# Optimization experiments

Measured on AMD Instinct MI355X. Metric: run time of the kernel, lower is better.

The kernel has to match this reference:

```python
import jax, jax.numpy as jnp
import numpy as np
import math

N_HEADS = 16
D_HEAD = 128
D_ROPE = 32
SPLIT = D_HEAD - D_ROPE  # 96
LATENT = 512
D_MODEL = 2048
B, T = 2, 2048


def _rotary_emb(num_tokens, d_rope):
    inv_freq = 1.0 / (10000.0 ** (jnp.arange(0, d_rope, 2, dtype=jnp.float32) / d_rope))
    t = jnp.arange(num_tokens, dtype=jnp.float32)
    freqs = jnp.einsum('t,f->tf', t, inv_freq)          # [T, d_rope/2]
    return jnp.concatenate([freqs, freqs], axis=-1)      # [T, d_rope]


def _apply_rotary(x, cos, sin):
    # x: [B,T,H,d_rope]; cos/sin: [1,T,1,d_rope]
    half = x.shape[-1] // 2
    x1, x2 = x[..., :half], x[..., half:]
    rot = jnp.concatenate([-x2, x1], axis=-1)
    return x * cos + rot * sin


def setup_inputs() -> dict:
    key = jax.random.key(0)
    ks = jax.random.split(key, 20)
    s = 0.02
    def w(k, i, o):
        return jax.random.normal(k, (i, o), dtype=jnp.float32) * s
    inp = {
        'input': jax.random.normal(ks[0], (B, T, D_MODEL), dtype=jnp.float32),
        'batch_size': B,
        'num_tokens': T,
        'Wdkv_w': w(ks[1], D_MODEL, LATENT), 'Wdkv_b': jnp.zeros((LATENT,), jnp.float32),
        'Wdq_w':  w(ks[2], D_MODEL, LATENT), 'Wdq_b':  jnp.zeros((LATENT,), jnp.float32),
        'Wuk_w':  w(ks[3], LATENT, N_HEADS * SPLIT),  'Wuk_b': jnp.zeros((N_HEADS * SPLIT,), jnp.float32),
        'Wuv_w':  w(ks[4], LATENT, N_HEADS * D_HEAD), 'Wuv_b': jnp.zeros((N_HEADS * D_HEAD,), jnp.float32),
        'Wuq_w':  w(ks[5], LATENT, N_HEADS * SPLIT),  'Wuq_b': jnp.zeros((N_HEADS * SPLIT,), jnp.float32),
        'Wqr_w':  w(ks[6], LATENT, N_HEADS * D_ROPE), 'Wqr_b': jnp.zeros((N_HEADS * D_ROPE,), jnp.float32),
        'Wkr_w':  w(ks[7], D_MODEL, N_HEADS * D_ROPE), 'Wkr_b': jnp.zeros((N_HEADS * D_ROPE,), jnp.float32),
        'Wo_w':   w(ks[8], N_HEADS * D_HEAD, D_MODEL), 'Wo_b': jnp.zeros((D_MODEL,), jnp.float32),
    }
    return inp


def reference(input, batch_size, num_tokens,
              Wdkv_w, Wdkv_b, Wdq_w, Wdq_b, Wuk_w, Wuk_b, Wuv_w, Wuv_b,
              Wuq_w, Wuq_b, Wqr_w, Wqr_b, Wkr_w, Wkr_b, Wo_w, Wo_b):
    lin = lambda x, w, b: x @ w + b
    bsz, T_ = batch_size, num_tokens

    c_kv = lin(input, Wdkv_w, Wdkv_b)                                   # [B,T,latent]
    k_base = lin(c_kv, Wuk_w, Wuk_b).reshape(bsz, T_, N_HEADS, SPLIT)
    v = lin(c_kv, Wuv_w, Wuv_b).reshape(bsz, T_, N_HEADS, D_HEAD)

    c_q = lin(input, Wdq_w, Wdq_b)
    q_base = lin(c_q, Wuq_w, Wuq_b).reshape(bsz, T_, N_HEADS, SPLIT)
    q_rot = lin(c_q, Wqr_w, Wqr_b).reshape(bsz, T_, N_HEADS, D_ROPE)

    emb = _rotary_emb(T_, D_ROPE)                                        # [T,d_rope]
    cos = jnp.cos(emb)[None, :, None, :]
    sin = jnp.sin(emb)[None, :, None, :]
    q_rot = _apply_rotary(q_rot, cos, sin)
    k_rot = _apply_rotary(lin(input, Wkr_w, Wkr_b).reshape(bsz, T_, N_HEADS, D_ROPE), cos, sin)

    q = jnp.concatenate([q_base, q_rot], axis=-1)                        # [B,T,H,d_head]
    k = jnp.concatenate([k_base, k_rot], axis=-1)

    scores = jnp.einsum('bqhd,bkhd->bhqk', q, k) / math.sqrt(D_HEAD)
    attn = jax.nn.softmax(scores, axis=-1)
    out = jnp.einsum('bhqk,bkhd->bqhd', attn, v)
    out = lin(out.reshape(bsz, T_, N_HEADS * D_HEAD), Wo_w, Wo_b)
    return out, c_kv, k_rot
```

## Files before the change

kernel.cpp:

```cpp
#include <hip/hip_runtime.h>

typedef __bf16 bf16x8 __attribute__((ext_vector_type(8)));
typedef float f32x4 __attribute__((ext_vector_type(4)));
typedef float f32x16 __attribute__((ext_vector_type(16)));

#define NROWS 4096
#define DM 2048
#define LAT 512
#define NH 16
#define DH 128

__device__ __forceinline__ unsigned short f2bf(float f) {
    union { float f; unsigned u; } v; v.f = f;
    unsigned r = v.u + 0x7fffu + ((v.u >> 16) & 1u);
    return (unsigned short)(r >> 16);
}
__device__ __forceinline__ void gload16(const void* g, void* l) {
    __builtin_amdgcn_global_load_lds((const __attribute__((address_space(1))) unsigned int*)g,
                                     (__attribute__((address_space(3))) unsigned int*)l, 16, 0, 0);
}
__device__ __forceinline__ unsigned cvtpk_bf16(float lo, float hi) {
    unsigned r;
    asm("v_cvt_pk_bf16_f32 %0, %1, %2" : "=v"(r) : "v"(lo), "v"(hi));
    return r;
}
__device__ __forceinline__ void pl32swap(unsigned& a, unsigned& b) {
    asm("v_permlane32_swap_b32 %0, %1" : "+v"(a), "+v"(b));
}
__device__ __forceinline__ float exp2a(float x) {
    float r;
    asm("v_exp_f32 %0, %1" : "=v"(r) : "v"(x));
    return r;
}

struct PrepParams {
    const float* tsrc[8]; unsigned short* tdst[8];
    int tK[8]; int tN[8]; int tstart[8];
    const float* input; unsigned short* xbf;
    float* cs; float* sn;
    const float* bsrc[8]; float* bdst[8]; int blen[8];
};

#define PREP_T_END   9984
#define PREP_X_END   18176
#define PREP_R_END   18304
#define PREP_B_END   18340

__global__ __launch_bounds__(256) void prep_kernel(PrepParams P) {
    const int bid = blockIdx.x, tid = threadIdx.x;
    if (bid < PREP_T_END) {
        int j = 0;
        #pragma unroll
        for (int i = 1; i < 8; ++i) if (bid >= P.tstart[i]) j = i;
        const int local = bid - P.tstart[j];
        const float* W = P.tsrc[j];
        unsigned short* Wt = P.tdst[j];
        const int K = P.tK[j], N = P.tN[j];
        const int nbx = N >> 5;
        const int nb = (local % nbx) * 32, kb = (local / nbx) * 32;
        __shared__ float tile[32][33];
        const int tx = tid & 31, ty = tid >> 5;
        #pragma unroll
        for (int i = 0; i < 32; i += 8)
            tile[ty + i][tx] = W[(size_t)(kb + ty + i) * N + nb + tx];
        __syncthreads();
        #pragma unroll
        for (int i = 0; i < 32; i += 8)
            Wt[(size_t)(nb + ty + i) * K + kb + tx] = f2bf(tile[tx][ty + i]);
    } else if (bid < PREP_X_END) {
        const int i = ((bid - PREP_T_END) * 256 + tid) * 4;
        float4 v = *(const float4*)(P.input + i);
        unsigned short* y = P.xbf + i;
        y[0] = f2bf(v.x); y[1] = f2bf(v.y); y[2] = f2bf(v.z); y[3] = f2bf(v.w);
    } else if (bid < PREP_R_END) {
        const int idx = (bid - PREP_X_END) * 256 + tid;
        const int i = idx & 15, t = idx >> 4;
        float inv = powf(10000.0f, -(float)i / 16.0f);
        float a = (float)t * inv;
        P.cs[idx] = cosf(a);
        P.sn[idx] = sinf(a);
    } else {
        const int gid = (bid - PREP_R_END) * 256 + tid;
        int off = 0;
        #pragma unroll
        for (int i = 0; i < 8; ++i) {
            if (gid >= off && gid < off + P.blen[i])
                P.bdst[i][gid - off] = P.bsrc[i][gid - off];
            off += P.blen[i];
        }
    }
}

__global__ __launch_bounds__(256) void gemm_fused_kernel(const unsigned short* __restrict__ A,
                                                         const unsigned short* __restrict__ Bt,
                                                         const float* __restrict__ biascat,
                                                         int K, int which,
                                                         float* __restrict__ outF,
                                                         unsigned short* __restrict__ outB0,
                                                         unsigned short* __restrict__ outB1,
                                                         unsigned short* __restrict__ outB0k,
                                                         float* __restrict__ outRope,
                                                         const float* __restrict__ cs,
                                                         const float* __restrict__ sn) {
    __shared__ __align__(16) unsigned short SM[2][8192];
    const int tid = threadIdx.x;
    const int mb = blockIdx.x * 128;
    const int by = blockIdx.y, nb = by * 128;
    const int w = tid >> 6, lane = tid & 63;
    const int wr = (w >> 1) * 64, wc = (w & 1) * 64;
    const int l15 = lane & 15, l4 = lane >> 4;
    const int srow = lane >> 2, sko = (lane & 3) * 8;

    f32x4 acc[4][4] = {};

    auto STAGE = [&](int buf, int k0) {
        #pragma unroll
        for (int c = 0; c < 16; c += 4) {
            int cc = c + w;
            if (cc < 8)
                gload16(A + (size_t)(mb + cc * 16 + srow) * K + k0 + sko, SM[buf] + cc * 512);
            else
                gload16(Bt + (size_t)(nb + (cc - 8) * 16 + srow) * K + k0 + sko, SM[buf] + 4096 + (cc - 8) * 512);
        }
    };

    const int nk = K >> 5;
    STAGE(0, 0);
    for (int kt = 0; kt < nk; ++kt) {
        const int buf = kt & 1;
        if (kt + 1 < nk) {
            STAGE(buf ^ 1, (kt + 1) << 5);
            asm volatile("s_waitcnt vmcnt(4)" ::: "memory");
        } else {
            asm volatile("s_waitcnt vmcnt(0)" ::: "memory");
        }
        __builtin_amdgcn_sched_barrier(0);
        __builtin_amdgcn_s_barrier();
        __builtin_amdgcn_sched_barrier(0);

        const unsigned short* As = SM[buf];
        const unsigned short* Bs = SM[buf] + 4096;
        bf16x8 af[4], bfr[4];
        #pragma unroll
        for (int mi = 0; mi < 4; ++mi)
            af[mi] = *(const bf16x8*)(As + (wr + mi * 16 + l15) * 32 + l4 * 8);
        #pragma unroll
        for (int ni = 0; ni < 4; ++ni)
            bfr[ni] = *(const bf16x8*)(Bs + (wc + ni * 16 + l15) * 32 + l4 * 8);
        #pragma unroll
        for (int mi = 0; mi < 4; ++mi)
            #pragma unroll
            for (int ni = 0; ni < 4; ++ni)
                acc[mi][ni] = __builtin_amdgcn_mfma_f32_16x16x32_bf16(af[mi], bfr[ni], acc[mi][ni], 0, 0, 0);
        __builtin_amdgcn_s_barrier();
    }

    if (which == 1 && by >= 12) {
        unsigned short* BT = &SM[0][0];
        const int c2b = nb - 1536;
        #pragma unroll
        for (int half = 0; half < 2; ++half) {
            __syncthreads();
            if ((wr >> 6) == half) {
                #pragma unroll
                for (int mi = 0; mi < 4; ++mi)
                    #pragma unroll
                    for (int ni = 0; ni < 4; ++ni) {
                        const int col = wc + ni * 16 + l15;
                        const float bv = biascat[nb + col];
                        ushort4 pv;
                        pv.x = f2bf(acc[mi][ni][0] + bv);
                        pv.y = f2bf(acc[mi][ni][1] + bv);
                        pv.z = f2bf(acc[mi][ni][2] + bv);
                        pv.w = f2bf(acc[mi][ni][3] + bv);
                        *(ushort4*)(BT + col * 72 + mi * 16 + l4 * 4) = pv;
                    }
            }
            __syncthreads();
            const int c = tid >> 1;
            #pragma unroll
            for (int j = 0; j < 4; ++j) {
                const int seg = (tid & 1) * 4 + j;
                uint4 val = *(const uint4*)(BT + c * 72 + seg * 8);
                *(uint4*)(outB1 + (size_t)(c2b + c) * 4096 + mb + half * 64 + seg * 8) = val;
            }
        }
        return;
    }

    #pragma unroll
    for (int mi = 0; mi < 4; ++mi) {
        const int row0 = mb + wr + mi * 16 + l4 * 4;
        #pragma unroll
        for (int ni = 0; ni < 4; ++ni) {
            const int colg = nb + wc + ni * 16 + l15;
            const float bv = biascat[colg];
            float v[4];
            #pragma unroll
            for (int r = 0; r < 4; ++r) v[r] = acc[mi][ni][r] + bv;

            if (which == 0) {
                if (by < 4) {
                    #pragma unroll
                    for (int r = 0; r < 4; ++r) {
                        outF[(size_t)(row0 + r) * 512 + colg] = v[r];
                        outB0[(size_t)(row0 + r) * 512 + colg] = f2bf(v[r]);
                    }
                } else if (by < 8) {
                    const int c2 = colg - 512;
                    #pragma unroll
                    for (int r = 0; r < 4; ++r)
                        outB1[(size_t)(row0 + r) * 512 + c2] = f2bf(v[r]);
                } else {
                    const int cloc = colg - 1024, i2 = cloc & 31, h2 = cloc >> 5;
                    const float pbv = biascat[colg ^ 16];
                    const bool lo = (ni & 1) == 0;
                    #pragma unroll
                    for (int r = 0; r < 4; ++r) {
                        float vp = acc[mi][ni ^ 1][r] + pbv;
                        int t = (row0 + r) & 2047;
                        float cc_ = cs[t * 16 + (i2 & 15)], ss_ = sn[t * 16 + (i2 & 15)];
                        float o = lo ? (v[r] * cc_ - vp * ss_) : (v[r] * cc_ + vp * ss_);
                        outRope[(size_t)(row0 + r) * 512 + cloc] = o;
                        outB0k[(size_t)(row0 + r) * 2048 + h2 * 128 + 96 + i2] = f2bf(o);
                    }
                }
            } else if (which == 1) {
                const int ocol = (colg / 96) * 128 + colg % 96;
                #pragma unroll
                for (int r = 0; r < 4; ++r)
                    outB0[(size_t)(row0 + r) * 2048 + ocol] = f2bf(v[r]);
            } else if (which == 2) {
                if (by < 12) {
                    const int ocol = (colg / 96) * 128 + colg % 96;
                    #pragma unroll
                    for (int r = 0; r < 4; ++r)
                        outB0[(size_t)(row0 + r) * 2048 + ocol] = f2bf(v[r]);
                } else {
                    const int cloc = colg - 1536, i2 = cloc & 31, h2 = cloc >> 5;
                    const float pbv = biascat[colg ^ 16];
                    const bool lo = (ni & 1) == 0;
                    #pragma unroll
                    for (int r = 0; r < 4; ++r) {
                        float vp = acc[mi][ni ^ 1][r] + pbv;
                        int t = (row0 + r) & 2047;
                        float cc_ = cs[t * 16 + (i2 & 15)], ss_ = sn[t * 16 + (i2 & 15)];
                        float o = lo ? (v[r] * cc_ - vp * ss_) : (v[r] * cc_ + vp * ss_);
                        outB0[(size_t)(row0 + r) * 2048 + h2 * 128 + 96 + i2] = f2bf(o);
                    }
                }
            } else {
                #pragma unroll
                for (int r = 0; r < 4; ++r)
                    outF[(size_t)(row0 + r) * 2048 + colg] = v[r];
            }
        }
    }
}

__global__ __launch_bounds__(256, 2) void attn_kernel(const unsigned short* __restrict__ Q,
                                                      const unsigned short* __restrict__ Kb,
                                                      const unsigned short* __restrict__ Vtg,
                                                      unsigned short* __restrict__ O) {
    __shared__ __align__(16) unsigned short Ks[2][64 * 128];
    __shared__ __align__(16) unsigned short Vs[2][128 * 64];

    const int tid = threadIdx.x, w = tid >> 6, lane = tid & 63;
    const int l31 = lane & 31, hi = lane >> 5;
    const int bid = blockIdx.x;
    const int logical = (bid & 7) * 64 + (bid >> 3);
    const int bh = logical >> 4, b = bh >> 4, h = bh & 15;
    const int qt = (logical & 15) * 128 + w * 32;
    const int qrow = qt + l31;
    const float sl2e = 0.08838834764831845f * 1.4426950408889634f;

    bf16x8 qf[8];
    const unsigned short* qptr = Q + (size_t)(b * 2048 + qrow) * 2048 + h * 128 + hi * 8;
    #pragma unroll
    for (int s = 0; s < 8; ++s) qf[s] = *(const bf16x8*)(qptr + s * 16);

    f32x16 acc[4] = {};
    float m_run = -1e30f, l_run = 0.0f;

    const int kl15 = lane >> 4, kd0 = lane & 15;
    const int vr = lane >> 3, vk = lane & 7;

    auto STAGE = [&](int buf, int kt) {
        #pragma unroll
        for (int i = 0; i < 4; ++i) {
            int c = w * 4 + i;
            int key = c * 4 + kl15;
            int d0 = (kd0 * 8) ^ ((key & 7) << 3);
            gload16(Kb + (size_t)(b * 2048 + kt + key) * 2048 + h * 128 + d0, &Ks[buf][c * 512]);
            int dv = c * 8 + vr;
            int k0 = (vk * 8) ^ ((dv & 7) << 3);
            gload16(Vtg + (size_t)(h * 128 + dv) * 4096 + b * 2048 + kt + k0, &Vs[buf][c * 512]);
        }
    };

    STAGE(0, 0);

    for (int t = 0; t < 32; ++t) {
        const int buf = t & 1;
        if (t < 31) {
            STAGE(buf ^ 1, (t + 1) * 64);
            asm volatile("s_waitcnt vmcnt(8)" ::: "memory");
        } else {
            asm volatile("s_waitcnt vmcnt(0)" ::: "memory");
        }
        __builtin_amdgcn_sched_barrier(0);
        __builtin_amdgcn_s_barrier();
        __builtin_amdgcn_sched_barrier(0);

        #pragma unroll
        for (int g = 0; g < 2; ++g) {
            const int key = g * 32 + l31;
            const unsigned short* kbase = &Ks[buf][key * 128];
            const int ksw = (key & 7) << 3;
            f32x16 sc = {};
            __builtin_amdgcn_s_setprio(1);
            #pragma unroll
            for (int s = 0; s < 8; ++s) {
                bf16x8 kf = *(const bf16x8*)(kbase + ((s * 16 + hi * 8) ^ ksw));
                sc = __builtin_amdgcn_mfma_f32_32x32x16_bf16(kf, qf[s], sc, 0, 0, 0);
            }
            __builtin_amdgcn_s_setprio(0);

            float t0 = fmaxf(sc[0], sc[1]),  t1 = fmaxf(sc[2], sc[3]);
            float t2 = fmaxf(sc[4], sc[5]),  t3 = fmaxf(sc[6], sc[7]);
            float t4 = fmaxf(sc[8], sc[9]),  t5 = fmaxf(sc[10], sc[11]);
            float t6 = fmaxf(sc[12], sc[13]), t7 = fmaxf(sc[14], sc[15]);
            float pm = fmaxf(fmaxf(fmaxf(t0, t1), fmaxf(t2, t3)),
                             fmaxf(fmaxf(t4, t5), fmaxf(t6, t7)));
            pm = fmaxf(pm, __shfl_xor(pm, 32, 64));

            if (__any(pm > m_run + 90.51f)) {
                float mn = fmaxf(m_run, pm);
                float f = exp2a((m_run - mn) * sl2e);
                m_run = mn;
                l_run *= f;
                #pragma unroll
                for (int dg = 0; dg < 4; ++dg)
                    #pragma unroll
                    for (int i = 0; i < 16; ++i) acc[dg][i] *= f;
            }
            const float mexp2 = m_run * sl2e;

            float e[16];
            #pragma unroll
            for (int j = 0; j < 16; ++j)
                e[j] = exp2a(fmaf(sc[j], sl2e, -mexp2));
            float a0 = e[0] + e[1], a1 = e[2] + e[3], a2 = e[4] + e[5], a3 = e[6] + e[7];
            float a4 = e[8] + e[9], a5 = e[10] + e[11], a6 = e[12] + e[13], a7 = e[14] + e[15];
            l_run += ((a0 + a1) + (a2 + a3)) + ((a4 + a5) + (a6 + a7));

            #pragma unroll
            for (int s2 = 0; s2 < 2; ++s2) {
                unsigned X0 = cvtpk_bf16(e[s2 * 8 + 0], e[s2 * 8 + 1]);
                unsigned X1 = cvtpk_bf16(e[s2 * 8 + 2], e[s2 * 8 + 3]);
                unsigned Y0 = cvtpk_bf16(e[s2 * 8 + 4], e[s2 * 8 + 5]);
                unsigned Y1 = cvtpk_bf16(e[s2 * 8 + 6], e[s2 * 8 + 7]);
                pl32swap(X0, Y0);
                pl32swap(X1, Y1);
                union { unsigned u[4]; bf16x8 v; } pf;
                pf.u[0] = X0; pf.u[1] = X1; pf.u[2] = Y0; pf.u[3] = Y1;

                const int kofs = g * 32 + s2 * 16 + hi * 8;
                __builtin_amdgcn_s_setprio(1);
                #pragma unroll
                for (int dg = 0; dg < 4; ++dg) {
                    const int d = dg * 32 + l31;
                    bf16x8 vf = *(const bf16x8*)(&Vs[buf][d * 64 + (kofs ^ ((d & 7) << 3))]);
                    acc[dg] = __builtin_amdgcn_mfma_f32_32x32x16_bf16(vf, pf.v, acc[dg], 0, 0, 0);
                }
                __builtin_amdgcn_s_setprio(0);
            }
        }
        __builtin_amdgcn_s_barrier();
    }

    l_run += __shfl_xor(l_run, 32, 64);
    const float inv = 1.0f / l_run;
    unsigned short* obase = O + (size_t)(b * 2048 + qrow) * 2048 + h * 128;
    #pragma unroll
    for (int dg = 0; dg < 4; ++dg)
        #pragma unroll
        for (int k = 0; k < 4; ++k) {
            ushort4 pv;
            pv.x = f2bf(acc[dg][4 * k + 0] * inv);
            pv.y = f2bf(acc[dg][4 * k + 1] * inv);
            pv.z = f2bf(acc[dg][4 * k + 2] * inv);
            pv.w = f2bf(acc[dg][4 * k + 3] * inv);
            *(ushort4*)(obase + dg * 32 + k * 8 + hi * 4) = pv;
        }
}

extern "C" void kernel_launch(void* const* d_in, const int* in_sizes, int n_in,
                              void* d_out, int out_size, void* d_ws, size_t ws_size,
                              hipStream_t stream) {
    (void)in_sizes; (void)n_in; (void)out_size; (void)ws_size;

    const float* input  = (const float*)d_in[0];
    const float* Wdkv_w = (const float*)d_in[3];
    const float* Wdkv_b = (const float*)d_in[4];
    const float* Wdq_w  = (const float*)d_in[5];
    const float* Wdq_b  = (const float*)d_in[6];
    const float* Wuk_w  = (const float*)d_in[7];
    const float* Wuk_b  = (const float*)d_in[8];
    const float* Wuv_w  = (const float*)d_in[9];
    const float* Wuv_b  = (const float*)d_in[10];
    const float* Wuq_w  = (const float*)d_in[11];
    const float* Wuq_b  = (const float*)d_in[12];
    const float* Wqr_w  = (const float*)d_in[13];
    const float* Wqr_b  = (const float*)d_in[14];
    const float* Wkr_w  = (const float*)d_in[15];
    const float* Wkr_b  = (const float*)d_in[16];
    const float* Wo_w   = (const float*)d_in[17];
    const float* Wo_b   = (const float*)d_in[18];

    float* out_main = (float*)d_out;
    float* out_ckv  = out_main + (size_t)NROWS * DM;
    float* out_krot = out_ckv + (size_t)NROWS * LAT;

    char* p = (char*)d_ws;
    auto alloc = [&](size_t bytes) { char* r = p; p += (bytes + 255) & ~(size_t)255; return r; };
    unsigned short* x_bf  = (unsigned short*)alloc((size_t)NROWS * DM * 2);
    unsigned short* w1_t  = (unsigned short*)alloc((size_t)1536 * DM * 2);
    unsigned short* w2_t  = (unsigned short*)alloc((size_t)3584 * LAT * 2);
    unsigned short* w3_t  = (unsigned short*)alloc((size_t)2048 * LAT * 2);
    unsigned short* w4_t  = (unsigned short*)alloc((size_t)DM * DM * 2);
    unsigned short* ckv_bf = (unsigned short*)alloc((size_t)NROWS * LAT * 2);
    unsigned short* cq_bf  = (unsigned short*)alloc((size_t)NROWS * LAT * 2);
    unsigned short* q_bf   = (unsigned short*)alloc((size_t)NROWS * DM * 2);
    unsigned short* k_bf   = (unsigned short*)alloc((size_t)NROWS * DM * 2);
    unsigned short* vt_g   = (unsigned short*)alloc((size_t)DM * NROWS * 2);
    unsigned short* ao_bf  = (unsigned short*)alloc((size_t)NROWS * DM * 2);
    float* cos_t = (float*)alloc((size_t)2048 * 16 * 4);
    float* sin_t = (float*)alloc((size_t)2048 * 16 * 4);
    float* bc1 = (float*)alloc(1536 * 4);
    float* bc2 = (float*)alloc(3584 * 4);
    float* bc3 = (float*)alloc(2048 * 4);
    float* bc4 = (float*)alloc(2048 * 4);

    PrepParams P;
    const float* tsrc[8] = {Wdkv_w, Wdq_w, Wkr_w, Wuk_w, Wuv_w, Wuq_w, Wqr_w, Wo_w};
    unsigned short* tdst[8] = {w1_t, w1_t + 512 * 2048, w1_t + 1024 * 2048,
                               w2_t, w2_t + 1536 * 512, w3_t, w3_t + 1536 * 512, w4_t};
    int tK[8] = {2048, 2048, 2048, 512, 512, 512, 512, 2048};
    int tN[8] = {512, 512, 512, 1536, 2048, 1536, 512, 2048};
    int tstart[8] = {0, 1024, 2048, 3072, 3840, 4864, 5632, 5888};
    const float* bsrc[8] = {Wdkv_b, Wdq_b, Wkr_b, Wuk_b, Wuv_b, Wuq_b, Wqr_b, Wo_b};
    float* bdst[8] = {bc1, bc1 + 512, bc1 + 1024, bc2, bc2 + 1536, bc3, bc3 + 1536, bc4};
    int blen[8] = {512, 512, 512, 1536, 2048, 1536, 512, 2048};
    for (int i = 0; i < 8; ++i) {
        P.tsrc[i] = tsrc[i]; P.tdst[i] = tdst[i]; P.tK[i] = tK[i]; P.tN[i] = tN[i];
        P.tstart[i] = tstart[i]; P.bsrc[i] = bsrc[i]; P.bdst[i] = bdst[i]; P.blen[i] = blen[i];
    }
    P.input = input; P.xbf = x_bf; P.cs = cos_t; P.sn = sin_t;
    prep_kernel<<<PREP_B_END, 256, 0, stream>>>(P);

    gemm_fused_kernel<<<dim3(32, 12), 256, 0, stream>>>(x_bf, w1_t, bc1, 2048, 0,
                                                        out_ckv, ckv_bf, cq_bf, k_bf, out_krot, cos_t, sin_t);
    gemm_fused_kernel<<<dim3(32, 28), 256, 0, stream>>>(ckv_bf, w2_t, bc2, 512, 1,
                                                        nullptr, k_bf, vt_g, nullptr, nullptr, nullptr, nullptr);
    gemm_fused_kernel<<<dim3(32, 16), 256, 0, stream>>>(cq_bf, w3_t, bc3, 512, 2,
                                                        nullptr, q_bf, nullptr, nullptr, nullptr, cos_t, sin_t);

    attn_kernel<<<512, 256, 0, stream>>>(q_bf, k_bf, vt_g, ao_bf);

    gemm_fused_kernel<<<dim3(32, 16), 256, 0, stream>>>(ao_bf, w4_t, bc4, 2048, 3,
                                                        out_main, nullptr, nullptr, nullptr, nullptr, nullptr, nullptr);
}
```

Baseline: 240.0 us.

## Merge up-projection GEMMs into one launch and use BK=64 for K=2048 GEMMs

Concatenates the Wuk/Wuv and Wuq/Wqr transposed weights into one buffer so the K- and Q-side up-projections run as a single 44-column-block launch. Blocks past column block 28 read from the c_q activation instead of c_kv. Separately templates the GEMM on BK and uses BK=64 for the K=2048 GEMMs to halve barrier and loop iterations. The merge removes one launch and improves occupancy, at the cost of doubled LDS for the BK=64 instances and more epilogue branching.

Measured after the change: 254.1 us. +5.9%, slower.

```diff
diff --git a/kernel.cpp b/kernel.cpp
--- a/kernel.cpp
+++ b/kernel.cpp
@@ -91,7 +91,9 @@
     }
 }
 
+template<int BK>
 __global__ __launch_bounds__(256) void gemm_fused_kernel(const unsigned short* __restrict__ A,
+                                                         const unsigned short* __restrict__ A2,
                                                          const unsigned short* __restrict__ Bt,
                                                          const float* __restrict__ biascat,
                                                          int K, int which,
@@ -102,35 +104,41 @@
                                                          float* __restrict__ outRope,
                                                          const float* __restrict__ cs,
                                                          const float* __restrict__ sn) {
-    __shared__ __align__(16) unsigned short SM[2][8192];
+    constexpr int RPC = 512 / BK;
+    constexpr int NCHA = BK / 4;
+    __shared__ __align__(16) unsigned short SM[2][256 * BK];
     const int tid = threadIdx.x;
     const int mb = blockIdx.x * 128;
     const int by = blockIdx.y, nb = by * 128;
     const int w = tid >> 6, lane = tid & 63;
     const int wr = (w >> 1) * 64, wc = (w & 1) * 64;
     const int l15 = lane & 15, l4 = lane >> 4;
-    const int srow = lane >> 2, sko = (lane & 3) * 8;
+    const int srow = lane / (BK / 8), sko = (lane % (BK / 8)) * 8;
+
+    const unsigned short* Ause = (which == 1 && by >= 28) ? A2 : A;
 
     f32x4 acc[4][4] = {};
 
     auto STAGE = [&](int buf, int k0) {
         #pragma unroll
-        for (int c = 0; c < 16; c += 4) {
+        for (int c = 0; c < 2 * NCHA; c += 4) {
             int cc = c + w;
-            if (cc < 8)
-                gload16(A + (size_t)(mb + cc * 16 + srow) * K + k0 + sko, SM[buf] + cc * 512);
+            if (cc < NCHA)
+                gload16(Ause + (size_t)(mb + cc * RPC + srow) * K + k0 + sko, SM[buf] + cc * 512);
             else
-                gload16(Bt + (size_t)(nb + (cc - 8) * 16 + srow) * K + k0 + sko, SM[buf] + 4096 + (cc - 8) * 512);
+                gload16(Bt + (size_t)(nb + (cc - NCHA) * RPC + srow) * K + k0 + sko,
+                        SM[buf] + 128 * BK + (cc - NCHA) * 512);
         }
     };
 
-    const int nk = K >> 5;
+    const int nk = K / BK;
     STAGE(0, 0);
     for (int kt = 0; kt < nk; ++kt) {
         const int buf = kt & 1;
         if (kt + 1 < nk) {
-            STAGE(buf ^ 1, (kt + 1) << 5);
-            asm volatile("s_waitcnt vmcnt(4)" ::: "memory");
+            STAGE(buf ^ 1, (kt + 1) * BK);
+            if constexpr (BK == 32) asm volatile("s_waitcnt vmcnt(4)" ::: "memory");
+            else                    asm volatile("s_waitcnt vmcnt(8)" ::: "memory");
         } else {
             asm volatile("s_waitcnt vmcnt(0)" ::: "memory");
         }
@@ -139,23 +147,26 @@
         __builtin_amdgcn_sched_barrier(0);
 
         const unsigned short* As = SM[buf];
-        const unsigned short* Bs = SM[buf] + 4096;
-        bf16x8 af[4], bfr[4];
-        #pragma unroll
-        for (int mi = 0; mi < 4; ++mi)
-            af[mi] = *(const bf16x8*)(As + (wr + mi * 16 + l15) * 32 + l4 * 8);
-        #pragma unroll
-        for (int ni = 0; ni < 4; ++ni)
-            bfr[ni] = *(const bf16x8*)(Bs + (wc + ni * 16 + l15) * 32 + l4 * 8);
-        #pragma unroll
-        for (int mi = 0; mi < 4; ++mi)
+        const unsigned short* Bs = SM[buf] + 128 * BK;
+        #pragma unroll
+        for (int kk = 0; kk < BK; kk += 32) {
+            bf16x8 af[4], bfr[4];
+            #pragma unroll
+            for (int mi = 0; mi < 4; ++mi)
+                af[mi] = *(const bf16x8*)(As + (wr + mi * 16 + l15) * BK + kk + l4 * 8);
             #pragma unroll
             for (int ni = 0; ni < 4; ++ni)
-                acc[mi][ni] = __builtin_amdgcn_mfma_f32_16x16x32_bf16(af[mi], bfr[ni], acc[mi][ni], 0, 0, 0);
+                bfr[ni] = *(const bf16x8*)(Bs + (wc + ni * 16 + l15) * BK + kk + l4 * 8);
+            #pragma unroll
+            for (int mi = 0; mi < 4; ++mi)
+                #pragma unroll
+                for (int ni = 0; ni < 4; ++ni)
+                    acc[mi][ni] = __builtin_amdgcn_mfma_f32_16x16x32_bf16(af[mi], bfr[ni], acc[mi][ni], 0, 0, 0);
+        }
         __builtin_amdgcn_s_barrier();
     }
 
-    if (which == 1 && by >= 12) {
+    if (which == 1 && by >= 12 && by < 28) {
         unsigned short* BT = &SM[0][0];
         const int c2b = nb - 1536;
         #pragma unroll
@@ -226,18 +237,19 @@
                     }
                 }
             } else if (which == 1) {
-                const int ocol = (colg / 96) * 128 + colg % 96;
-                #pragma unroll
-                for (int r = 0; r < 4; ++r)
-                    outB0[(size_t)(row0 + r) * 2048 + ocol] = f2bf(v[r]);
-            } else if (which == 2) {
                 if (by < 12) {
                     const int ocol = (colg / 96) * 128 + colg % 96;
                     #pragma unroll
                     for (int r = 0; r < 4; ++r)
                         outB0[(size_t)(row0 + r) * 2048 + ocol] = f2bf(v[r]);
+                } else if (by < 40) {
+                    const int c3 = colg - 3584;
+                    const int ocol = (c3 / 96) * 128 + c3 % 96;
+                    #pragma unroll
+                    for (int r = 0; r < 4; ++r)
+                        outB0k[(size_t)(row0 + r) * 2048 + ocol] = f2bf(v[r]);
                 } else {
-                    const int cloc = colg - 1536, i2 = cloc & 31, h2 = cloc >> 5;
+                    const int cloc = colg - 5120, i2 = cloc & 31, h2 = cloc >> 5;
                     const float pbv = biascat[colg ^ 16];
                     const bool lo = (ni & 1) == 0;
                     #pragma unroll
@@ -246,7 +258,7 @@
                         int t = (row0 + r) & 2047;
                         float cc_ = cs[t * 16 + (i2 & 15)], ss_ = sn[t * 16 + (i2 & 15)];
                         float o = lo ? (v[r] * cc_ - vp * ss_) : (v[r] * cc_ + vp * ss_);
-                        outB0[(size_t)(row0 + r) * 2048 + h2 * 128 + 96 + i2] = f2bf(o);
+                        outB0k[(size_t)(row0 + r) * 2048 + h2 * 128 + 96 + i2] = f2bf(o);
                     }
                 }
             } else {
@@ -426,8 +438,7 @@
     auto alloc = [&](size_t bytes) { char* r = p; p += (bytes + 255) & ~(size_t)255; return r; };
     unsigned short* x_bf  = (unsigned short*)alloc((size_t)NROWS * DM * 2);
     unsigned short* w1_t  = (unsigned short*)alloc((size_t)1536 * DM * 2);
-    unsigned short* w2_t  = (unsigned short*)alloc((size_t)3584 * LAT * 2);
-    unsigned short* w3_t  = (unsigned short*)alloc((size_t)2048 * LAT * 2);
+    unsigned short* w23_t = (unsigned short*)alloc((size_t)5632 * LAT * 2);
     unsigned short* w4_t  = (unsigned short*)alloc((size_t)DM * DM * 2);
     unsigned short* ckv_bf = (unsigned short*)alloc((size_t)NROWS * LAT * 2);
     unsigned short* cq_bf  = (unsigned short*)alloc((size_t)NROWS * LAT * 2);
@@ -437,20 +448,19 @@
     unsigned short* ao_bf  = (unsigned short*)alloc((size_t)NROWS * DM * 2);
     float* cos_t = (float*)alloc((size_t)2048 * 16 * 4);
     float* sin_t = (float*)alloc((size_t)2048 * 16 * 4);
-    float* bc1 = (float*)alloc(1536 * 4);
-    float* bc2 = (float*)alloc(3584 * 4);
-    float* bc3 = (float*)alloc(2048 * 4);
-    float* bc4 = (float*)alloc(2048 * 4);
+    float* bc1  = (float*)alloc(1536 * 4);
+    float* bc23 = (float*)alloc(5632 * 4);
+    float* bc4  = (float*)alloc(2048 * 4);
 
     PrepParams P;
     const float* tsrc[8] = {Wdkv_w, Wdq_w, Wkr_w, Wuk_w, Wuv_w, Wuq_w, Wqr_w, Wo_w};
     unsigned short* tdst[8] = {w1_t, w1_t + 512 * 2048, w1_t + 1024 * 2048,
-                               w2_t, w2_t + 1536 * 512, w3_t, w3_t + 1536 * 512, w4_t};
+                               w23_t, w23_t + 1536 * 512, w23_t + 3584 * 512, w23_t + 5120 * 512, w4_t};
     int tK[8] = {2048, 2048, 2048, 512, 512, 512, 512, 2048};
     int tN[8] = {512, 512, 512, 1536, 2048, 1536, 512, 2048};
     int tstart[8] = {0, 1024, 2048, 3072, 3840, 4864, 5632, 5888};
     const float* bsrc[8] = {Wdkv_b, Wdq_b, Wkr_b, Wuk_b, Wuv_b, Wuq_b, Wqr_b, Wo_b};
-    float* bdst[8] = {bc1, bc1 + 512, bc1 + 1024, bc2, bc2 + 1536, bc3, bc3 + 1536, bc4};
+    float* bdst[8] = {bc1, bc1 + 512, bc1 + 1024, bc23, bc23 + 1536, bc23 + 3584, bc23 + 5120, bc4};
     int blen[8] = {512, 512, 512, 1536, 2048, 1536, 512, 2048};
     for (int i = 0; i < 8; ++i) {
         P.tsrc[i] = tsrc[i]; P.tdst[i] = tdst[i]; P.tK[i] = tK[i]; P.tN[i] = tN[i];
@@ -459,15 +469,13 @@
     P.input = input; P.xbf = x_bf; P.cs = cos_t; P.sn = sin_t;
     prep_kernel<<<PREP_B_END, 256, 0, stream>>>(P);
 
-    gemm_fused_kernel<<<dim3(32, 12), 256, 0, stream>>>(x_bf, w1_t, bc1, 2048, 0,
-                                                        out_ckv, ckv_bf, cq_bf, k_bf, out_krot, cos_t, sin_t);
-    gemm_fused_kernel<<<dim3(32, 28), 256, 0, stream>>>(ckv_bf, w2_t, bc2, 512, 1,
-                                                        nullptr, k_bf, vt_g, nullptr, nullptr, nullptr, nullptr);
-    gemm_fused_kernel<<<dim3(32, 16), 256, 0, stream>>>(cq_bf, w3_t, bc3, 512, 2,
-                                                        nullptr, q_bf, nullptr, nullptr, nullptr, cos_t, sin_t);
+    gemm_fused_kernel<64><<<dim3(32, 12), 256, 0, stream>>>(x_bf, nullptr, w1_t, bc1, 2048, 0,
+                                                            out_ckv, ckv_bf, cq_bf, k_bf, out_krot, cos_t, sin_t);
+    gemm_fused_kernel<32><<<dim3(32, 44), 256, 0, stream>>>(ckv_bf, cq_bf, w23_t, bc23, 512, 1,
+                                                            nullptr, k_bf, vt_g, q_bf, nullptr, cos_t, sin_t);
 
     attn_kernel<<<512, 256, 0, stream>>>(q_bf, k_bf, vt_g, ao_bf);
 
-    gemm_fused_kernel<<<dim3(32, 16), 256, 0, stream>>>(ao_bf, w4_t, bc4, 2048, 3,
-                                                        out_main, nullptr, nullptr, nullptr, nullptr, nullptr, nullptr);
-}
+    gemm_fused_kernel<64><<<dim3(32, 16), 256, 0, stream>>>(ao_bf, nullptr, w4_t, bc4, 2048, 3,
+                                                            out_main, nullptr, nullptr, nullptr, nullptr, nullptr, nullptr);
+}
```
